# Kernel optimization log

Measured on AMD Instinct MI355X. Metric: run time of the kernel, lower is better.

## Reference

```python
import jax, jax.numpy as jnp
import numpy as np

HIDDEN = 128   # hidden_dim == input_dim (embedding feeds LSTMCell directly)
OUT = 200000   # output_dim: item catalog size
T = 64         # num_timesteps
K = 50         # num_recommendations
HIST = 200     # length of user history x


def setup_inputs() -> dict:
    key = jax.random.key(0)
    ks = jax.random.split(key, 6)
    s = 0.02
    return {
        "x": jax.random.randint(ks[0], (HIST,), 1, OUT + 1),  # 1-indexed items
        "embed_table": jax.random.normal(ks[1], (OUT, HIDDEN), jnp.float32) * s,
        "W_ih": jax.random.normal(ks[2], (4 * HIDDEN, HIDDEN), jnp.float32) * s,
        "W_hh": jax.random.normal(ks[3], (4 * HIDDEN, HIDDEN), jnp.float32) * s,
        "b_ih": jnp.zeros((4 * HIDDEN,), jnp.float32),
        "b_hh": jnp.zeros((4 * HIDDEN,), jnp.float32),
        "W_out": jax.random.normal(ks[4], (OUT, HIDDEN), jnp.float32) * s,
        "b_out": jnp.zeros((OUT,), jnp.float32),
    }


def reference(x, embed_table, W_ih, W_hh, b_ih, b_hh, W_out, b_out):
    # Faithful translation of RecModel.forward with prev_a_hat=None, prev_feedback=None.
    def step(carry, i):
        h, c, mask, a_hat, feedback = carry
        # at i==0 the embedding input is forced to zeros (feedback starts at 0 anyway)
        emb = jnp.where(i > 0, embed_table[a_hat] * feedback.astype(jnp.float32), 0.0)
        # LSTMCell: gates order (input, forget, cell, output) as in torch
        gates = W_ih @ emb + b_ih + W_hh @ h + b_hh
        ig, fg, gg, og = jnp.split(gates, 4)
        c_new = jax.nn.sigmoid(fg) * c + jax.nn.sigmoid(ig) * jnp.tanh(gg)
        h_new = jax.nn.sigmoid(og) * jnp.tanh(c_new)
        probs = jax.nn.softmax(W_out @ h_new + b_out)  # Softmax(dim=0) on [OUT]
        masked = probs * mask
        _, top_items = jax.lax.top_k(masked, K)
        hit = jnp.isin(top_items + 1, x)               # x is 1-indexed
        any_hit = jnp.any(hit)
        first_hit = top_items[jnp.argmax(hit)]         # first intersecting item
        a_new = jnp.where(any_hit, first_hit, top_items[0]).astype(jnp.int32)
        fb_new = jnp.where(any_hit, 1, -1).astype(jnp.int32)
        mask_new = mask.at[a_new].set(0.0)
        return (h_new, c_new, mask_new, a_new, fb_new), (a_new, fb_new, masked)

    init = (
        jnp.zeros((HIDDEN,), jnp.float32),
        jnp.zeros((HIDDEN,), jnp.float32),
        jnp.ones((OUT,), jnp.float32),
        jnp.array(0, jnp.int32),
        jnp.array(0, jnp.int32),
    )
    _, (a_hats, feedbacks, masked_probs) = jax.lax.scan(step, init, jnp.arange(T))
    return a_hats, feedbacks, masked_probs
```

## Files before the change

kernel.cpp:

```cpp
#include <hip/hip_runtime.h>
#include <stdint.h>

#define OUTN   200000
#define HID    128
#define NSTEP  64
#define KTOP   50
#define NBINS  1024
#define CAP    4096
#define NBLK   256
#define NTHR   512
#define NWRD   6250
#define GRP    8
#define GSZ    32
#define SLOTS  64

__device__ __forceinline__ float    gldf(const float* p){ return __hip_atomic_load(p, __ATOMIC_RELAXED, __HIP_MEMORY_SCOPE_AGENT); }
__device__ __forceinline__ void     gstf(float* p, float v){ __hip_atomic_store(p, v, __ATOMIC_RELAXED, __HIP_MEMORY_SCOPE_AGENT); }
__device__ __forceinline__ unsigned gldu(const unsigned* p){ return __hip_atomic_load(p, __ATOMIC_RELAXED, __HIP_MEMORY_SCOPE_AGENT); }
__device__ __forceinline__ void     gstu(unsigned* p, unsigned v){ __hip_atomic_store(p, v, __ATOMIC_RELAXED, __HIP_MEMORY_SCOPE_AGENT); }
__device__ __forceinline__ unsigned long long gld64(const unsigned long long* p){ return __hip_atomic_load(p, __ATOMIC_RELAXED, __HIP_MEMORY_SCOPE_AGENT); }
__device__ __forceinline__ void     gst64(unsigned long long* p, unsigned long long v){ __hip_atomic_store(p, v, __ATOMIC_RELAXED, __HIP_MEMORY_SCOPE_AGENT); }

__device__ __forceinline__ float dot128f(const float* __restrict__ w, const float* __restrict__ h){
  const float4* w4 = (const float4*)w;
  float acc = 0.f;
  #pragma unroll
  for (int k=0;k<32;k++){
    float4 q = w4[k];
    const float* hp = h + k*4;
    acc += q.x*hp[0] + q.y*hp[1] + q.z*hp[2] + q.w*hp[3];
  }
  return acc;
}

__device__ __forceinline__ int binOf(float l, float rlo, float rsc){
  float b = (l - rlo) * rsc;
  b = fminf(fmaxf(b, 0.f), (float)(NBINS-1));
  return (int)b;
}

__device__ __forceinline__ void blockRed3(float& mx, float& mn, float& a, int tid, float* sm ){
  __syncthreads();
  #pragma unroll
  for (int o=32;o;o>>=1){
    mx=fmaxf(mx,__shfl_xor(mx,o)); mn=fminf(mn,__shfl_xor(mn,o));
    a+=__shfl_xor(a,o);
  }
  if ((tid&63)==0){ int w=tid>>6; sm[w*3+0]=mx; sm[w*3+1]=mn; sm[w*3+2]=a; }
  __syncthreads();
  if (tid==0){
    for (int k=1;k<8;k++){
      sm[0]=fmaxf(sm[0],sm[k*3+0]); sm[1]=fminf(sm[1],sm[k*3+1]); sm[2]+=sm[k*3+2];
    }
  }
  __syncthreads();
  mx=sm[0]; mn=sm[1]; a=sm[2];
}

__device__ __forceinline__ void blockRedPair(float& p, int& i, int tid, float* smp, int* smi){
  __syncthreads();
  #pragma unroll
  for (int o=32;o;o>>=1){
    float p2=__shfl_xor(p,o); int i2=__shfl_xor(i,o);
    if (p2>p || (p2==p && i2<i)){ p=p2; i=i2; }
  }
  if ((tid&63)==0){ smp[tid>>6]=p; smi[tid>>6]=i; }
  __syncthreads();
  if (tid==0){
    for (int k=1;k<8;k++){
      if (smp[k]>smp[0] || (smp[k]==smp[0] && smi[k]<smi[0])){ smp[0]=smp[k]; smi[0]=smi[k]; }
    }
  }
  __syncthreads();
  p=smp[0]; i=smi[0];
}

__device__ __forceinline__ int blockRedSum(int v, int tid, int* smi){
  __syncthreads();
  #pragma unroll
  for (int o=32;o;o>>=1) v += __shfl_xor(v,o);
  if ((tid&63)==0) smi[tid>>6]=v;
  __syncthreads();
  if (tid==0){ int s=0; for(int k=0;k<8;k++) s+=smi[k]; smi[0]=s; }
  __syncthreads();
  return smi[0];
}

__device__ __forceinline__ void histSelect(unsigned* histL, unsigned* csum, int tid, int K, int* outp){
  int base = NBINS - 2*(tid+1);
  csum[tid] = histL[base] + histL[base+1];
  __syncthreads();
  for (int off=1; off<NTHR; off<<=1){
    unsigned add = (tid>=off) ? csum[tid-off] : 0u;
    __syncthreads();
    csum[tid] += add;
    __syncthreads();
  }
  unsigned pre = (tid==0)?0u:csum[tid-1];
  if (csum[tid] >= (unsigned)K && pre < (unsigned)K){
    unsigned run = pre; int bs = base;
    for (int b=base+1; b>=base; --b){
      run += histL[b];
      if (run >= (unsigned)K){ bs=b; break; }
    }
    outp[0]=bs; outp[1]=(int)run;
  }
  if (tid==NTHR-1 && csum[tid] < (unsigned)K){ outp[0]=0; outp[1]=(int)csum[tid]; }
  __syncthreads();
}

__device__ __forceinline__ void gsync(unsigned* garr, unsigned* gctr, unsigned* grel,
                                      int bid, unsigned s){
  asm volatile("s_waitcnt vmcnt(0) lgkmcnt(0)" ::: "memory");
  __syncthreads();
  if (threadIdx.x==0){
    int g = bid>>5;
    unsigned r = __hip_atomic_fetch_add(garr+g*64, 1u, __ATOMIC_RELAXED, __HIP_MEMORY_SCOPE_AGENT);
    if (r == s*GSZ-1u){
      unsigned q = __hip_atomic_fetch_add(gctr, 1u, __ATOMIC_RELAXED, __HIP_MEMORY_SCOPE_AGENT);
      if (q == s*GRP-1u){
        #pragma unroll
        for (int k=0;k<GRP;k++)
          __hip_atomic_store(grel+k*64, s, __ATOMIC_RELAXED, __HIP_MEMORY_SCOPE_AGENT);
      }
    }
    while (__hip_atomic_load(grel+g*64, __ATOMIC_RELAXED, __HIP_MEMORY_SCOPE_AGENT) < s)
      __builtin_amdgcn_s_sleep(2);
  }
  __syncthreads();
  asm volatile("" ::: "memory");
}

extern "C" __global__ void k_init(const int* __restrict__ x,
                                  const float* __restrict__ b_ih, const float* __restrict__ b_hh,
                                  unsigned* mask_bits, unsigned* inx_bits,
                                  float* pubInv, float* h_ws, float* c_ws,
                                  unsigned* garr, unsigned* gctr, unsigned* grel)
{
  int tid = threadIdx.x;
  for (int i=tid;i<NWRD;i+=1024){ mask_bits[i]=0xFFFFFFFFu; inx_bits[i]=0u; }
  for (int i=tid;i<GRP*64;i+=1024){ garr[i]=0u; grel[i]=0u; }
  if (tid<64) gctr[tid]=0u;
  if (tid==0) pubInv[0]=0.f;
  if (tid<HID){
    float ig=b_ih[tid]       +b_hh[tid];
    float gg=b_ih[tid+2*HID] +b_hh[tid+2*HID];
    float og=b_ih[tid+3*HID] +b_hh[tid+3*HID];
    float si=1.f/(1.f+expf(-ig)), so=1.f/(1.f+expf(-og));
    float cn=si*tanhf(gg);
    c_ws[tid]=cn; h_ws[tid]=so*tanhf(cn);
  }
  __syncthreads();
  if (tid<200){
    int v = x[tid]-1;
    if (v>=0 && v<OUTN) atomicOr(&inx_bits[v>>5], 1u<<(v&31));
  }
}

struct FusedP {
  const float* emb;  const float* Wih;  const float* Whh;
  const float* bih;  const float* bhh;  const float* Wout; const float* bout;
  float* out;
  float* l_ws; float* partials;
  unsigned* mask_bits; unsigned* inx_bits;
  unsigned* cntb; unsigned long long* cand;
  float* pubInv; float* h_ws; float* c_ws;
  unsigned* garr; unsigned* gctr; unsigned* grel;
};

extern "C" __global__ void __launch_bounds__(NTHR) k_fused(FusedP p)
{
  __shared__ float    h_l[HID];
  __shared__ float    emb_l[HID];
  __shared__ float    gates[4*HID];
  __shared__ float    c_l[HID];
  __shared__ unsigned m_l[32];
  __shared__ unsigned hl[NBINS];
  __shared__ unsigned csum[NTHR];
  __shared__ unsigned cnt_l[NBLK];
  __shared__ float    smf[24];
  __shared__ float    smp[8];
  __shared__ int      smi[8];
  __shared__ int      s_sel[2];
  __shared__ int      s_nc, s_cnt, s_flag;

  const int tid=threadIdx.x, bid=blockIdx.x;
  const int start = bid*781 + (bid<64 ? bid : 64);
  const int cnt   = 781 + (bid<64 ? 1 : 0);
  const int w_lo  = start>>5;
  const int nw    = ((start+cnt-1)>>5) - w_lo + 1;
  unsigned bs = 0;

  if (bid==0 && tid<HID) c_l[tid]=gldf(&p.c_ws[tid]);

  float lv0=0.f, lv1=0.f; unsigned mv0=0u, mv1=0u;

  for (int t=0; t<NSTEP; ++t){
    if (tid<HID) h_l[tid]=gldf(&p.h_ws[tid]);
    if (tid<nw)  m_l[tid]=gldu(&p.mask_bits[w_lo+tid]);
    for (int i=tid;i<NBINS;i+=NTHR) hl[i]=0u;
    const float invSp = gldf(p.pubInv);
    __syncthreads();

    float mx=-3e38f, mn=3e38f, se=0.f;
    float* orowp = p.out + 2*NSTEP + (size_t)(t-1)*OUTN;
    {
      int j=tid;
      if (j<cnt){
        int row=start+j;
        if (t>0) __builtin_nontemporal_store(mv0 ? expf(lv0)*invSp : 0.f, &orowp[row]);
        float l = dot128f(p.Wout+(size_t)row*HID, h_l) + p.bout[row];
        gstf(&p.l_ws[row], l);
        lv0=l; se += expf(l)-1.f;
        mv0 = (m_l[(row>>5)-w_lo]>>(row&31))&1u;
        if (mv0){ mx=fmaxf(mx,l); mn=fminf(mn,l); }
      } else { mv0=0u; }
      j=tid+NTHR;
      if (j<cnt){
        int row=start+j;
        if (t>0) __builtin_nontemporal_store(mv1 ? expf(lv1)*invSp : 0.f, &orowp[row]);
        float l = dot128f(p.Wout+(size_t)row*HID, h_l) + p.bout[row];
        gstf(&p.l_ws[row], l);
        lv1=l; se += expf(l)-1.f;
        mv1 = (m_l[(row>>5)-w_lo]>>(row&31))&1u;
        if (mv1){ mx=fmaxf(mx,l); mn=fminf(mn,l); }
      } else { mv1=0u; }
    }
    blockRed3(mx,mn,se,tid,smf);
    if (tid==0){ float* q=&p.partials[bid*4]; gstf(q,mx); gstf(q+1,mn); gstf(q+2,se); }

    const bool okloc = (mx>mn);
    if (okloc){
      const float rsc=(float)NBINS/(mx-mn);
      if (mv0) atomicAdd(&hl[binOf(lv0,mn,rsc)],1u);
      if (mv1) atomicAdd(&hl[binOf(lv1,mn,rsc)],1u);
      if (tid==0){ s_cnt=0; s_sel[0]=NBINS; s_sel[1]=0; }
      __syncthreads();
      histSelect(hl,csum,tid,KTOP,s_sel);
      const int bstar=s_sel[0];
      if (mv0 && binOf(lv0,mn,rsc)>=bstar){
        int pos=atomicAdd(&s_cnt,1);
        if (pos<SLOTS){
          int row=start+tid;
          gst64(&p.cand[bid*SLOTS+pos],
                ((unsigned long long)__float_as_uint(lv0)<<32)|(unsigned)row);
        }
      }
      if (mv1 && binOf(lv1,mn,rsc)>=bstar){
        int pos=atomicAdd(&s_cnt,1);
        if (pos<SLOTS){
          int row=start+tid+NTHR;
          gst64(&p.cand[bid*SLOTS+pos],
                ((unsigned long long)__float_as_uint(lv1)<<32)|(unsigned)row);
        }
      }
      __syncthreads();
      if (tid==0) gstu(&p.cntb[bid],(unsigned)s_cnt);
    } else {
      if (tid==0) gstu(&p.cntb[bid],0x7fffffffu);
    }
    ++bs; gsync(p.garr,p.gctr,p.grel,bid,bs);

    if (bid==0){
      float gmx=-3e38f,gmn=3e38f,gse=0.f;
      if (tid<NBLK){
        const float* q=&p.partials[tid*4];
        gmx=gldf(q); gmn=gldf(q+1); gse=gldf(q+2);
        cnt_l[tid]=gldu(&p.cntb[tid]);
      }
      blockRed3(gmx,gmn,gse,tid,smf);
      const float invS = 1.f/(2.0e5f+gse);
      if (tid==0) s_flag=0;
      __syncthreads();
      if (tid<NBLK && cnt_l[tid]>SLOTS) s_flag=1;
      __syncthreads();
      int a, fb;
      if (!s_flag){
        unsigned long long sv[32]; unsigned um=0u;
        #pragma unroll
        for (int k=0;k<32;k++){
          int j=tid+k*NTHR; int b=j>>6, s=j&63;
          if (s < (int)cnt_l[b]){ sv[k]=gld64(&p.cand[j]); um|=1u<<k; }
          else sv[k]=0ull;
        }
        float bp=-3.4e38f; int bi=0x7fffffff;
        float hp=-3.4e38f; int hidx=0x7fffffff;
        #pragma unroll
        for (int k=0;k<32;k++){
          if ((um>>k)&1u){
            int idx=(int)(unsigned)(sv[k]&0xffffffffu);
            float l=__uint_as_float((unsigned)(sv[k]>>32));
            if (l>bp || (l==bp && idx<bi)){ bp=l; bi=idx; }
            if (((p.inx_bits[idx>>5]>>(idx&31))&1u) && (l>hp || (l==hp && idx<hidx))){ hp=l; hidx=idx; }
          }
        }
        blockRedPair(bp,bi,tid,smp,smi);
        blockRedPair(hp,hidx,tid,smp,smi);
        if (hidx != 0x7fffffff){
          int better=0;
          #pragma unroll
          for (int k=0;k<32;k++){
            if ((um>>k)&1u){
              int idx=(int)(unsigned)(sv[k]&0xffffffffu);
              float l=__uint_as_float((unsigned)(sv[k]>>32));
              better += (l>hp || (l==hp && idx<hidx)) ? 1 : 0;
            }
          }
          better=blockRedSum(better,tid,smi);
          if (better<KTOP){ a=hidx; fb=1; } else { a=bi; fb=-1; }
        } else { a=bi; fb=-1; }
      } else {
        unsigned* candf=(unsigned*)p.cand;
        int nc;
        if (gmn>=gmx){
          unsigned w=gldu(&p.mask_bits[tid]);
          hl[tid]=w; csum[tid]=(unsigned)__popc(w);
          __syncthreads();
          for (int off=1; off<NTHR; off<<=1){
            unsigned add=(tid>=off)?csum[tid-off]:0u;
            __syncthreads();
            csum[tid]+=add;
            __syncthreads();
          }
          unsigned pre = tid? csum[tid-1]:0u;
          if (pre<(unsigned)KTOP){
            unsigned word=hl[tid]; unsigned r=pre;
            for (int b2=0;b2<32 && r<(unsigned)KTOP;b2++){
              if ((word>>b2)&1u){ gstu(&candf[r],(unsigned)(tid*32+b2)); r++; }
            }
          }
          __syncthreads();
          nc = (int)(csum[NTHR-1]<(unsigned)KTOP ? csum[NTHR-1] : (unsigned)KTOP);
        } else {
          for (int i=tid;i<NBINS;i+=NTHR) hl[i]=0u;
          if (tid==0){ s_sel[0]=NBINS; s_sel[1]=0; }
          __syncthreads();
          const float sc2=(float)NBINS/(gmx-gmn);
          for (int i=tid;i<OUTN;i+=NTHR)
            if ((gldu(&p.mask_bits[i>>5])>>(i&31))&1u)
              atomicAdd(&hl[binOf(gldf(&p.l_ws[i]),gmn,sc2)],1u);
          __syncthreads();
          histSelect(hl,csum,tid,KTOP,s_sel);
          int b2=s_sel[0], c2=s_sel[1];
          if (c2<=CAP){
            if (tid==0) s_cnt=0;
            __syncthreads();
            for (int i=tid;i<OUTN;i+=NTHR){
              if ((gldu(&p.mask_bits[i>>5])>>(i&31))&1u && binOf(gldf(&p.l_ws[i]),gmn,sc2)>=b2){
                int q=atomicAdd(&s_cnt,1);
                if (q<CAP) gstu(&candf[q],(unsigned)i);
              }
            }
            __syncthreads();
            nc = (s_cnt<CAP ? s_cnt : CAP);
          } else {
            if (tid==0){
              int c=0;
              for (int i=0;i<OUTN && c<KTOP;i++)
                if (((gldu(&p.mask_bits[i>>5])>>(i&31))&1u) && binOf(gldf(&p.l_ws[i]),gmn,sc2)>=b2)
                  gstu(&candf[c++],(unsigned)i);
              s_nc=c;
            }
            __syncthreads();
            nc=s_nc;
          }
        }
        float bp=-3.4e38f; int bi=0x7fffffff;
        float hp=-3.4e38f; int hidx=0x7fffffff;
        for (int j=tid;j<nc;j+=NTHR){
          int idx=(int)gldu(&candf[j]);
          float l=gldf(&p.l_ws[idx]);
          if (l>bp || (l==bp && idx<bi)){ bp=l; bi=idx; }
          if (((p.inx_bits[idx>>5]>>(idx&31))&1u) && (l>hp || (l==hp && idx<hidx))){ hp=l; hidx=idx; }
        }
        blockRedPair(bp,bi,tid,smp,smi);
        blockRedPair(hp,hidx,tid,smp,smi);
        if (hidx != 0x7fffffff){
          int better=0;
          for (int j=tid;j<nc;j+=NTHR){
            int idx=(int)gldu(&candf[j]);
            float l=gldf(&p.l_ws[idx]);
            better += (l>hp || (l==hp && idx<hidx)) ? 1 : 0;
          }
          better=blockRedSum(better,tid,smi);
          if (better<KTOP){ a=hidx; fb=1; } else { a=bi; fb=-1; }
        } else { a=bi; fb=-1; }
      }
      if (a<0 || a>=OUTN) a=0;

      if (tid==0){
        p.out[t]       = (float)a;
        p.out[NSTEP+t] = (float)fb;
        atomicAnd(&p.mask_bits[a>>5], ~(1u<<(a&31)));
        gstf(p.pubInv, invS);
      }
      if (tid<HID) emb_l[tid]=p.emb[(size_t)a*HID+tid]*(float)fb;
      __syncthreads();
      float g = dot128f(p.Wih+(size_t)tid*HID, emb_l) + dot128f(p.Whh+(size_t)tid*HID, h_l)
              + p.bih[tid] + p.bhh[tid];
      gates[tid]=g;
      __syncthreads();
      if (tid<HID){
        float ig=gates[tid], fg=gates[tid+HID], gg=gates[tid+2*HID], og=gates[tid+3*HID];
        float si=1.f/(1.f+expf(-ig)), sf=1.f/(1.f+expf(-fg)), so=1.f/(1.f+expf(-og));
        float cn=sf*c_l[tid]+si*tanhf(gg);
        float hn=so*tanhf(cn);
        c_l[tid]=cn; gstf(&p.h_ws[tid],hn);
      }
    }
    ++bs; gsync(p.garr,p.gctr,p.grel,bid,bs);
  }

  {
    const float invSL = gldf(p.pubInv);
    float* orow = p.out + 2*NSTEP + (size_t)(NSTEP-1)*OUTN;
    int j=tid;
    if (j<cnt){ int row=start+j; __builtin_nontemporal_store(mv0 ? expf(lv0)*invSL : 0.f, &orow[row]); }
    j=tid+NTHR;
    if (j<cnt){ int row=start+j; __builtin_nontemporal_store(mv1 ? expf(lv1)*invSL : 0.f, &orow[row]); }
  }
}

extern "C" void kernel_launch(void* const* d_in, const int* in_sizes, int n_in,
                              void* d_out, int out_size, void* d_ws, size_t ws_size,
                              hipStream_t stream)
{
  const int*   x    = (const int*)d_in[0];
  const float* emb  = (const float*)d_in[1];
  const float* Wih  = (const float*)d_in[2];
  const float* Whh  = (const float*)d_in[3];
  const float* bih  = (const float*)d_in[4];
  const float* bhh  = (const float*)d_in[5];
  const float* Wout = (const float*)d_in[6];
  const float* bout = (const float*)d_in[7];
  float* out = (float*)d_out;

  char* ws = (char*)d_ws;
  float*    l_ws      = (float*)(ws + 0);
  float*    partials  = (float*)(ws + 800256);
  unsigned* mask_bits = (unsigned*)(ws + 804352);
  unsigned* inx_bits  = (unsigned*)(ws + 829440);
  unsigned* cntb      = (unsigned*)(ws + 854528);
  unsigned long long* cand = (unsigned long long*)(ws + 855552);
  unsigned* garr      = (unsigned*)(ws + 986624);
  unsigned* gctr      = (unsigned*)(ws + 988672);
  unsigned* grel      = (unsigned*)(ws + 988928);
  float*    pubInv    = (float*)(ws + 990976);
  float*    h_ws      = (float*)(ws + 991232);
  float*    c_ws      = (float*)(ws + 991744);

  hipLaunchKernelGGL(k_init, dim3(1), dim3(1024), 0, stream,
                     x, bih, bhh, mask_bits, inx_bits, pubInv, h_ws, c_ws, garr, gctr, grel);

  FusedP p;
  p.emb=emb; p.Wih=Wih; p.Whh=Whh; p.bih=bih; p.bhh=bhh; p.Wout=Wout; p.bout=bout;
  p.out=out; p.l_ws=l_ws; p.partials=partials;
  p.mask_bits=mask_bits; p.inx_bits=inx_bits;
  p.cntb=cntb; p.cand=cand;
  p.pubInv=pubInv; p.h_ws=h_ws; p.c_ws=c_ws;
  p.garr=garr; p.gctr=gctr; p.grel=grel;

  void* args[] = { &p };
  hipLaunchCooperativeKernel((const void*)k_fused, dim3(NBLK), dim3(NTHR), args, 0, stream);
}
```

Before: 5.133 ms.

## Use coalesced wave-cooperative GEMV, flat grid barrier, sentinel-padded candidate slots

The per-thread 128-float row dot product over W_out is replaced by a wave-cooperative scheme. Half-waves read one row with coalesced float4 loads, reduce with shuffles, and each lane keeps its own result, so every wave owns 98 contiguous rows. The LSTM gate GEMV is rewritten the same way. The two-level hierarchical grid barrier becomes a single atomic counter with a monotonically increasing target. Unused candidate slots are filled with a sentinel, so block 0 can scan all slots without count-mask bookkeeping, at the cost of extra shuffle reductions and more contention on one atomic.

```diff
diff --git a/kernel.cpp b/kernel.cpp
--- a/kernel.cpp
+++ b/kernel.cpp
@@ -10,9 +10,8 @@
 #define NBLK   256
 #define NTHR   512
 #define NWRD   6250
-#define GRP    8
-#define GSZ    32
 #define SLOTS  64
+#define SENT   0xFF80000000000000ull
 
 __device__ __forceinline__ float    gldf(const float* p){ return __hip_atomic_load(p, __ATOMIC_RELAXED, __HIP_MEMORY_SCOPE_AGENT); }
 __device__ __forceinline__ void     gstf(float* p, float v){ __hip_atomic_store(p, v, __ATOMIC_RELAXED, __HIP_MEMORY_SCOPE_AGENT); }
@@ -21,18 +20,6 @@
 __device__ __forceinline__ unsigned long long gld64(const unsigned long long* p){ return __hip_atomic_load(p, __ATOMIC_RELAXED, __HIP_MEMORY_SCOPE_AGENT); }
 __device__ __forceinline__ void     gst64(unsigned long long* p, unsigned long long v){ __hip_atomic_store(p, v, __ATOMIC_RELAXED, __HIP_MEMORY_SCOPE_AGENT); }
 
-__device__ __forceinline__ float dot128f(const float* __restrict__ w, const float* __restrict__ h){
-  const float4* w4 = (const float4*)w;
-  float acc = 0.f;
-  #pragma unroll
-  for (int k=0;k<32;k++){
-    float4 q = w4[k];
-    const float* hp = h + k*4;
-    acc += q.x*hp[0] + q.y*hp[1] + q.z*hp[2] + q.w*hp[3];
-  }
-  return acc;
-}
-
 __device__ __forceinline__ int binOf(float l, float rlo, float rsc){
   float b = (l - rlo) * rsc;
   b = fminf(fmaxf(b, 0.f), (float)(NBINS-1));
@@ -109,22 +96,12 @@
   __syncthreads();
 }
 
-__device__ __forceinline__ void gsync(unsigned* garr, unsigned* gctr, unsigned* grel,
-                                      int bid, unsigned s){
+__device__ __forceinline__ void gsync(unsigned* bar, unsigned target){
   asm volatile("s_waitcnt vmcnt(0) lgkmcnt(0)" ::: "memory");
   __syncthreads();
   if (threadIdx.x==0){
-    int g = bid>>5;
-    unsigned r = __hip_atomic_fetch_add(garr+g*64, 1u, __ATOMIC_RELAXED, __HIP_MEMORY_SCOPE_AGENT);
-    if (r == s*GSZ-1u){
-      unsigned q = __hip_atomic_fetch_add(gctr, 1u, __ATOMIC_RELAXED, __HIP_MEMORY_SCOPE_AGENT);
-      if (q == s*GRP-1u){
-        #pragma unroll
-        for (int k=0;k<GRP;k++)
-          __hip_atomic_store(grel+k*64, s, __ATOMIC_RELAXED, __HIP_MEMORY_SCOPE_AGENT);
-      }
-    }
-    while (__hip_atomic_load(grel+g*64, __ATOMIC_RELAXED, __HIP_MEMORY_SCOPE_AGENT) < s)
+    __hip_atomic_fetch_add(bar, 1u, __ATOMIC_RELAXED, __HIP_MEMORY_SCOPE_AGENT);
+    while (__hip_atomic_load(bar, __ATOMIC_RELAXED, __HIP_MEMORY_SCOPE_AGENT) < target)
       __builtin_amdgcn_s_sleep(2);
   }
   __syncthreads();
@@ -134,14 +111,11 @@
 extern "C" __global__ void k_init(const int* __restrict__ x,
                                   const float* __restrict__ b_ih, const float* __restrict__ b_hh,
                                   unsigned* mask_bits, unsigned* inx_bits,
-                                  float* pubInv, float* h_ws, float* c_ws,
-                                  unsigned* garr, unsigned* gctr, unsigned* grel)
+                                  float* pubInv, float* h_ws, float* c_ws, unsigned* bar)
 {
   int tid = threadIdx.x;
   for (int i=tid;i<NWRD;i+=1024){ mask_bits[i]=0xFFFFFFFFu; inx_bits[i]=0u; }
-  for (int i=tid;i<GRP*64;i+=1024){ garr[i]=0u; grel[i]=0u; }
-  if (tid<64) gctr[tid]=0u;
-  if (tid==0) pubInv[0]=0.f;
+  if (tid==0){ pubInv[0]=0.f; *bar=0u; }
   if (tid<HID){
     float ig=b_ih[tid]       +b_hh[tid];
     float gg=b_ih[tid+2*HID] +b_hh[tid+2*HID];
@@ -164,20 +138,18 @@
   float* l_ws; float* partials;
   unsigned* mask_bits; unsigned* inx_bits;
   unsigned* cntb; unsigned long long* cand;
-  float* pubInv; float* h_ws; float* c_ws;
-  unsigned* garr; unsigned* gctr; unsigned* grel;
+  float* pubInv; float* h_ws; float* c_ws; unsigned* bar;
 };
 
 extern "C" __global__ void __launch_bounds__(NTHR) k_fused(FusedP p)
 {
-  __shared__ float    h_l[HID];
-  __shared__ float    emb_l[HID];
+  __shared__ __align__(16) float h_l[HID];
+  __shared__ __align__(16) float emb_l[HID];
   __shared__ float    gates[4*HID];
   __shared__ float    c_l[HID];
   __shared__ unsigned m_l[32];
   __shared__ unsigned hl[NBINS];
   __shared__ unsigned csum[NTHR];
-  __shared__ unsigned cnt_l[NBLK];
   __shared__ float    smf[24];
   __shared__ float    smp[8];
   __shared__ int      smi[8];
@@ -185,46 +157,77 @@
   __shared__ int      s_nc, s_cnt, s_flag;
 
   const int tid=threadIdx.x, bid=blockIdx.x;
+  const int wv=tid>>6, lane=tid&63;
   const int start = bid*781 + (bid<64 ? bid : 64);
   const int cnt   = 781 + (bid<64 ? 1 : 0);
   const int w_lo  = start>>5;
   const int nw    = ((start+cnt-1)>>5) - w_lo + 1;
-  unsigned bs = 0;
+  const int wbase = start + wv*98;
+  const int wrows = min(98, start+cnt-wbase);
+  const int nB    = wrows-64;
+  const int rA    = wbase + lane;
+  const int rB    = wbase + 64 + lane;
+  unsigned barT = 0;
 
   if (bid==0 && tid<HID) c_l[tid]=gldf(&p.c_ws[tid]);
 
-  float lv0=0.f, lv1=0.f; unsigned mv0=0u, mv1=0u;
+  float lvA=0.f, lvB=0.f; unsigned mvA=0u, mvB=0u;
 
   for (int t=0; t<NSTEP; ++t){
     if (tid<HID) h_l[tid]=gldf(&p.h_ws[tid]);
     if (tid<nw)  m_l[tid]=gldu(&p.mask_bits[w_lo+tid]);
     for (int i=tid;i<NBINS;i+=NTHR) hl[i]=0u;
     const float invSp = gldf(p.pubInv);
+    if (tid==0){ s_cnt=0; s_sel[0]=NBINS; s_sel[1]=0; }
     __syncthreads();
 
+    if (t>0){
+      float* orowp = p.out + 2*NSTEP + (size_t)(t-1)*OUTN;
+      __builtin_nontemporal_store(mvA ? expf(lvA)*invSp : 0.f, &orowp[rA]);
+      if (lane<nB) __builtin_nontemporal_store(mvB ? expf(lvB)*invSp : 0.f, &orowp[rB]);
+    }
+
+    const float4 hreg = *(const float4*)&h_l[(lane&31)*4];
+
+    #pragma unroll 4
+    for (int b=0;b<32;b++){
+      int r = wbase + 2*b + (lane>>5);
+      const float4 q = *(const float4*)(p.Wout + (size_t)r*HID + ((lane&31)<<2));
+      float s = q.x*hreg.x + q.y*hreg.y + q.z*hreg.z + q.w*hreg.w;
+      #pragma unroll
+      for (int o=16;o;o>>=1) s += __shfl_xor(s,o);
+      float sel = __shfl(s, (lane&1)<<5);
+      if ((lane>>1)==b) lvA = sel;
+    }
+    lvA += p.bout[rA];
+    mvA = (m_l[(rA>>5)-w_lo]>>(rA&31))&1u;
+    gstf(&p.l_ws[rA], lvA);
+
+    #pragma unroll 4
+    for (int b=0;b<17;b++){
+      int off = 64 + 2*b + (lane>>5);
+      float s = 0.f;
+      if (off < wrows){
+        const float4 q = *(const float4*)(p.Wout + (size_t)(wbase+off)*HID + ((lane&31)<<2));
+        s = q.x*hreg.x + q.y*hreg.y + q.z*hreg.z + q.w*hreg.w;
+      }
+      #pragma unroll
+      for (int o=16;o;o>>=1) s += __shfl_xor(s,o);
+      float sel = __shfl(s, (lane&1)<<5);
+      if ((lane>>1)==b && lane<nB) lvB = sel;
+    }
+    if (lane<nB){
+      lvB += p.bout[rB];
+      mvB = (m_l[(rB>>5)-w_lo]>>(rB&31))&1u;
+      gstf(&p.l_ws[rB], lvB);
+    } else mvB=0u;
+
     float mx=-3e38f, mn=3e38f, se=0.f;
-    float* orowp = p.out + 2*NSTEP + (size_t)(t-1)*OUTN;
-    {
-      int j=tid;
-      if (j<cnt){
-        int row=start+j;
-        if (t>0) __builtin_nontemporal_store(mv0 ? expf(lv0)*invSp : 0.f, &orowp[row]);
-        float l = dot128f(p.Wout+(size_t)row*HID, h_l) + p.bout[row];
-        gstf(&p.l_ws[row], l);
-        lv0=l; se += expf(l)-1.f;
-        mv0 = (m_l[(row>>5)-w_lo]>>(row&31))&1u;
-        if (mv0){ mx=fmaxf(mx,l); mn=fminf(mn,l); }
-      } else { mv0=0u; }
-      j=tid+NTHR;
-      if (j<cnt){
-        int row=start+j;
-        if (t>0) __builtin_nontemporal_store(mv1 ? expf(lv1)*invSp : 0.f, &orowp[row]);
-        float l = dot128f(p.Wout+(size_t)row*HID, h_l) + p.bout[row];
-        gstf(&p.l_ws[row], l);
-        lv1=l; se += expf(l)-1.f;
-        mv1 = (m_l[(row>>5)-w_lo]>>(row&31))&1u;
-        if (mv1){ mx=fmaxf(mx,l); mn=fminf(mn,l); }
-      } else { mv1=0u; }
+    se += expf(lvA)-1.f;
+    if (mvA){ mx=fmaxf(mx,lvA); mn=fminf(mn,lvA); }
+    if (lane<nB){
+      se += expf(lvB)-1.f;
+      if (mvB){ mx=fmaxf(mx,lvB); mn=fminf(mn,lvB); }
     }
     blockRed3(mx,mn,se,tid,smf);
     if (tid==0){ float* q=&p.partials[bid*4]; gstf(q,mx); gstf(q+1,mn); gstf(q+2,se); }
@@ -232,79 +235,65 @@
     const bool okloc = (mx>mn);
     if (okloc){
       const float rsc=(float)NBINS/(mx-mn);
-      if (mv0) atomicAdd(&hl[binOf(lv0,mn,rsc)],1u);
-      if (mv1) atomicAdd(&hl[binOf(lv1,mn,rsc)],1u);
-      if (tid==0){ s_cnt=0; s_sel[0]=NBINS; s_sel[1]=0; }
+      if (mvA) atomicAdd(&hl[binOf(lvA,mn,rsc)],1u);
+      if (mvB) atomicAdd(&hl[binOf(lvB,mn,rsc)],1u);
       __syncthreads();
       histSelect(hl,csum,tid,KTOP,s_sel);
       const int bstar=s_sel[0];
-      if (mv0 && binOf(lv0,mn,rsc)>=bstar){
+      if (mvA && binOf(lvA,mn,rsc)>=bstar){
         int pos=atomicAdd(&s_cnt,1);
-        if (pos<SLOTS){
-          int row=start+tid;
+        if (pos<SLOTS)
           gst64(&p.cand[bid*SLOTS+pos],
-                ((unsigned long long)__float_as_uint(lv0)<<32)|(unsigned)row);
-        }
-      }
-      if (mv1 && binOf(lv1,mn,rsc)>=bstar){
+                ((unsigned long long)__float_as_uint(lvA)<<32)|(unsigned)rA);
+      }
+      if (mvB && binOf(lvB,mn,rsc)>=bstar){
         int pos=atomicAdd(&s_cnt,1);
-        if (pos<SLOTS){
-          int row=start+tid+NTHR;
+        if (pos<SLOTS)
           gst64(&p.cand[bid*SLOTS+pos],
-                ((unsigned long long)__float_as_uint(lv1)<<32)|(unsigned)row);
-        }
+                ((unsigned long long)__float_as_uint(lvB)<<32)|(unsigned)rB);
       }
       __syncthreads();
       if (tid==0) gstu(&p.cntb[bid],(unsigned)s_cnt);
+      for (int i=s_cnt+tid;i<SLOTS;i+=NTHR) gst64(&p.cand[bid*SLOTS+i], SENT);
     } else {
       if (tid==0) gstu(&p.cntb[bid],0x7fffffffu);
     }
-    ++bs; gsync(p.garr,p.gctr,p.grel,bid,bs);
+    barT += NBLK; gsync(p.bar, barT);
 
     if (bid==0){
-      float gmx=-3e38f,gmn=3e38f,gse=0.f;
+      float gmx=-3e38f,gmn=3e38f,gse=0.f; unsigned cl=0u;
       if (tid<NBLK){
         const float* q=&p.partials[tid*4];
         gmx=gldf(q); gmn=gldf(q+1); gse=gldf(q+2);
-        cnt_l[tid]=gldu(&p.cntb[tid]);
-      }
+        cl=gldu(&p.cntb[tid]);
+      }
+      if (tid==0) s_flag=0;
       blockRed3(gmx,gmn,gse,tid,smf);
+      if (cl>SLOTS) s_flag=1;
+      __syncthreads();
       const float invS = 1.f/(2.0e5f+gse);
-      if (tid==0) s_flag=0;
-      __syncthreads();
-      if (tid<NBLK && cnt_l[tid]>SLOTS) s_flag=1;
-      __syncthreads();
       int a, fb;
       if (!s_flag){
-        unsigned long long sv[32]; unsigned um=0u;
-        #pragma unroll
-        for (int k=0;k<32;k++){
-          int j=tid+k*NTHR; int b=j>>6, s=j&63;
-          if (s < (int)cnt_l[b]){ sv[k]=gld64(&p.cand[j]); um|=1u<<k; }
-          else sv[k]=0ull;
-        }
         float bp=-3.4e38f; int bi=0x7fffffff;
         float hp=-3.4e38f; int hidx=0x7fffffff;
-        #pragma unroll
+        #pragma unroll 8
         for (int k=0;k<32;k++){
-          if ((um>>k)&1u){
-            int idx=(int)(unsigned)(sv[k]&0xffffffffu);
-            float l=__uint_as_float((unsigned)(sv[k]>>32));
-            if (l>bp || (l==bp && idx<bi)){ bp=l; bi=idx; }
-            if (((p.inx_bits[idx>>5]>>(idx&31))&1u) && (l>hp || (l==hp && idx<hidx))){ hp=l; hidx=idx; }
-          }
+          unsigned long long v = gld64(&p.cand[tid + k*NTHR]);
+          int idx=(int)(unsigned)(v&0xffffffffu);
+          float l=__uint_as_float((unsigned)(v>>32));
+          if (l>bp || (l==bp && idx<bi)){ bp=l; bi=idx; }
+          if (((p.inx_bits[idx>>5]>>(idx&31))&1u) && (l>hp || (l==hp && idx<hidx))){ hp=l; hidx=idx; }
         }
         blockRedPair(bp,bi,tid,smp,smi);
         blockRedPair(hp,hidx,tid,smp,smi);
         if (hidx != 0x7fffffff){
           int better=0;
-          #pragma unroll
+          #pragma unroll 8
           for (int k=0;k<32;k++){
-            if ((um>>k)&1u){
-              int idx=(int)(unsigned)(sv[k]&0xffffffffu);
-              float l=__uint_as_float((unsigned)(sv[k]>>32));
-              better += (l>hp || (l==hp && idx<hidx)) ? 1 : 0;
-            }
+            unsigned long long v = gld64(&p.cand[tid + k*NTHR]);
+            int idx=(int)(unsigned)(v&0xffffffffu);
+            float l=__uint_as_float((unsigned)(v>>32));
+            better += (l>hp || (l==hp && idx<hidx)) ? 1 : 0;
           }
           better=blockRedSum(better,tid,smi);
           if (better<KTOP){ a=hidx; fb=1; } else { a=bi; fb=-1; }
@@ -396,9 +385,25 @@
       }
       if (tid<HID) emb_l[tid]=p.emb[(size_t)a*HID+tid]*(float)fb;
       __syncthreads();
-      float g = dot128f(p.Wih+(size_t)tid*HID, emb_l) + dot128f(p.Whh+(size_t)tid*HID, h_l)
-              + p.bih[tid] + p.bhh[tid];
-      gates[tid]=g;
+      {
+        const float4 er=*(const float4*)&emb_l[(lane&31)*4];
+        const float4 hr=*(const float4*)&h_l[(lane&31)*4];
+        float gv=0.f;
+        #pragma unroll 4
+        for (int b=0;b<32;b++){
+          int g=(wv<<6)+2*b+(lane>>5);
+          const float4 qi=*(const float4*)(p.Wih+(size_t)g*HID+((lane&31)<<2));
+          const float4 qh=*(const float4*)(p.Whh+(size_t)g*HID+((lane&31)<<2));
+          float s=qi.x*er.x+qi.y*er.y+qi.z*er.z+qi.w*er.w
+                + qh.x*hr.x+qh.y*hr.y+qh.z*hr.z+qh.w*hr.w;
+          #pragma unroll
+          for (int o=16;o;o>>=1) s+=__shfl_xor(s,o);
+          float sel=__shfl(s,(lane&1)<<5);
+          if ((lane>>1)==b) gv=sel;
+        }
+        int g=(wv<<6)+lane;
+        gates[g]=gv+p.bih[g]+p.bhh[g];
+      }
       __syncthreads();
       if (tid<HID){
         float ig=gates[tid], fg=gates[tid+HID], gg=gates[tid+2*HID], og=gates[tid+3*HID];
@@ -408,16 +413,14 @@
         c_l[tid]=cn; gstf(&p.h_ws[tid],hn);
       }
     }
-    ++bs; gsync(p.garr,p.gctr,p.grel,bid,bs);
+    barT += NBLK; gsync(p.bar, barT);
   }
 
   {
     const float invSL = gldf(p.pubInv);
     float* orow = p.out + 2*NSTEP + (size_t)(NSTEP-1)*OUTN;
-    int j=tid;
-    if (j<cnt){ int row=start+j; __builtin_nontemporal_store(mv0 ? expf(lv0)*invSL : 0.f, &orow[row]); }
-    j=tid+NTHR;
-    if (j<cnt){ int row=start+j; __builtin_nontemporal_store(mv1 ? expf(lv1)*invSL : 0.f, &orow[row]); }
+    __builtin_nontemporal_store(mvA ? expf(lvA)*invSL : 0.f, &orow[rA]);
+    if (lane<nB) __builtin_nontemporal_store(mvB ? expf(lvB)*invSL : 0.f, &orow[rB]);
   }
 }
 
@@ -442,23 +445,20 @@
   unsigned* inx_bits  = (unsigned*)(ws + 829440);
   unsigned* cntb      = (unsigned*)(ws + 854528);
   unsigned long long* cand = (unsigned long long*)(ws + 855552);
-  unsigned* garr      = (unsigned*)(ws + 986624);
-  unsigned* gctr      = (unsigned*)(ws + 988672);
-  unsigned* grel      = (unsigned*)(ws + 988928);
-  float*    pubInv    = (float*)(ws + 990976);
-  float*    h_ws      = (float*)(ws + 991232);
-  float*    c_ws      = (float*)(ws + 991744);
+  unsigned* bar       = (unsigned*)(ws + 986624);
+  float*    pubInv    = (float*)(ws + 986880);
+  float*    h_ws      = (float*)(ws + 987136);
+  float*    c_ws      = (float*)(ws + 987648);
 
   hipLaunchKernelGGL(k_init, dim3(1), dim3(1024), 0, stream,
-                     x, bih, bhh, mask_bits, inx_bits, pubInv, h_ws, c_ws, garr, gctr, grel);
+                     x, bih, bhh, mask_bits, inx_bits, pubInv, h_ws, c_ws, bar);
 
   FusedP p;
   p.emb=emb; p.Wih=Wih; p.Whh=Whh; p.bih=bih; p.bhh=bhh; p.Wout=Wout; p.bout=bout;
   p.out=out; p.l_ws=l_ws; p.partials=partials;
   p.mask_bits=mask_bits; p.inx_bits=inx_bits;
   p.cntb=cntb; p.cand=cand;
-  p.pubInv=pubInv; p.h_ws=h_ws; p.c_ws=c_ws;
-  p.garr=garr; p.gctr=gctr; p.grel=grel;
+  p.pubInv=pubInv; p.h_ws=h_ws; p.c_ws=c_ws; p.bar=bar;
 
   void* args[] = { &p };
   hipLaunchCooperativeKernel((const void*)k_fused, dim3(NBLK), dim3(NTHR), args, 0, stream);
```

Result: slower. 5.808 ms (+13.1%).
